# Performance work log

Measured on AMD Instinct MI355X. Metric: run time of the kernel, lower is better.

The kernel has to match this reference:

```python
import jax, jax.numpy as jnp
import numpy as np
jax.config.update('jax_enable_x64', True)

T = 524288      # hash table size (2^19)
D = 3           # input_dim
F = 2           # feature_dim
L = 16          # levels
N_MIN, N_MAX = 16, 512
B = 262144      # batch of query points
V = 2 ** D      # voxel corners

_b = np.exp((np.log(N_MAX) - np.log(N_MIN)) / (L - 1))
RESOLUTIONS = jnp.asarray(np.floor(N_MIN * _b ** np.arange(L)).astype(np.int64)).reshape(1, 1, L, 1)
PRIMES = jnp.asarray(np.array([1, 2654435761, 805459861], dtype=np.int64))
_border = np.empty((D, V), dtype=np.int64)
for i in range(D):
    _border[i, :] = np.array(([0] * 2 ** i + [1] * 2 ** i) * 2 ** (D - i - 1), dtype=np.int64)
BORDER_ADDS = jnp.asarray(_border).reshape(1, D, 1, V)


def setup_inputs() -> dict:
    key = jax.random.key(0)
    kx, kt = jax.random.split(key)
    x = jax.random.uniform(kx, (B, D), dtype=jnp.float32)  # coords in [0,1)
    # nn.Embedding init: uniform(-1e-4, 1e-4) per level
    tables = jax.random.uniform(kt, (L, T, F), dtype=jnp.float32, minval=-1e-4, maxval=1e-4)
    return {"x": x, "tables": tables}


def reference(x, tables):
    # scale to each grid resolution: (B, D, L, 1)
    scaled = x[:, :, None, None] * RESOLUTIONS.astype(x.dtype)
    # voxel corner integer coords: (B, D, L, V)
    grid = jnp.floor(scaled).astype(jnp.int64) + BORDER_ADDS
    # NVIDIA fast hash: xor of coord*prime over dims, mod T -> (B, L, V)
    hashed = grid * PRIMES.reshape(1, D, 1, 1)
    idx = jnp.remainder(jnp.bitwise_xor(jnp.bitwise_xor(hashed[:, 0], hashed[:, 1]), hashed[:, 2]), T)
    # gather per-level features: (B, L, V, F)
    feats = tables[jnp.arange(L)[None, :, None], idx]
    # multilinear interpolation weights: prod over dims -> (B, L, V)
    w = jnp.prod(1.0 - jnp.abs(scaled - grid.astype(scaled.dtype)), axis=1)
    # weighted corner sum -> (B, L, F) -> (B, L*F)
    out = jnp.einsum('blv,blvf->blf', w, feats)
    return out.reshape(x.shape[0], L * F)
```

## Files before the change

kernel.cpp:

```cpp
#include <hip/hip_runtime.h>


constexpr int      kT      = 524288;
constexpr unsigned kMask   = kT - 1;
constexpr int      kB      = 262144;
constexpr unsigned kP1     = 2654435761u;
constexpr unsigned kP2     = 805459861u;
constexpr int      kBins   = 4096;
constexpr int      kCap    = 128;
constexpr int      kOvfCap = 65536;

typedef float f32x4 __attribute__((ext_vector_type(4)));

__device__ __forceinline__ unsigned morton12(float x0, float x1, float x2) {
    unsigned a = min(15u, (unsigned)(x0 * 16.0f));
    unsigned b = min(15u, (unsigned)(x1 * 16.0f));
    unsigned c = min(15u, (unsigned)(x2 * 16.0f));
    unsigned key = 0;
#pragma unroll
    for (int i = 3; i >= 0; --i)
        key = (key << 3) | (((a >> i) & 1u) << 2) | (((b >> i) & 1u) << 1) | ((c >> i) & 1u);
    return key;
}

__device__ __forceinline__ void hashenc_body(const float x0, const float x1, const float x2,
                                             const f32x4* __restrict__ tab4base,
                                             f32x4* __restrict__ out, const unsigned sid) {
    f32x4 o[8];
    constexpr float kResF[16] = {16, 20, 25, 32, 40, 50, 64, 80,
                                 101, 128, 161, 203, 256, 322, 406, 512};
#pragma unroll
    for (int l = 0; l < 16; ++l) {
        const float res = kResF[l];
        const float s0 = x0 * res, s1 = x1 * res, s2 = x2 * res;
        const float f0 = floorf(s0), f1 = floorf(s1), f2 = floorf(s2);
        const float r0 = s0 - f0, r1 = s1 - f1, r2 = s2 - f2;
        const unsigned c0 = (unsigned)f0;
        const unsigned h1a = (unsigned)f1 * kP1, h1b = h1a + kP1;
        const unsigned h2a = (unsigned)f2 * kP2, h2b = h2a + kP2;
        const float w0a = 1.0f - r0, w1a = 1.0f - r1, w2a = 1.0f - r2;
        const f32x4* __restrict__ tab4 = tab4base + (size_t)l * (kT / 2);
        float a0 = 0.0f, a1 = 0.0f;
#pragma unroll
        for (int q = 0; q < 4; ++q) {
            const unsigned g = ((q & 1) ? h1b : h1a) ^ ((q & 2) ? h2b : h2a);
            const unsigned i0 = (c0 ^ g) & kMask;
            const unsigned i1 = ((c0 + 1u) ^ g) & kMask;
            const f32x4 A = tab4[i0 >> 1];
            const f32x4 B = tab4[i1 >> 1];
            const float p0x = (i0 & 1) ? A.z : A.x;
            const float p0y = (i0 & 1) ? A.w : A.y;
            const float p1x = (i1 & 1) ? B.z : B.x;
            const float p1y = (i1 & 1) ? B.w : B.y;
            const float wyz = ((q & 1) ? r1 : w1a) * ((q & 2) ? r2 : w2a);
            const float wl = wyz * w0a;
            const float wr = wyz * r0;
            a0 = fmaf(wl, p0x, fmaf(wr, p1x, a0));
            a1 = fmaf(wl, p0y, fmaf(wr, p1y, a1));
        }
        if (l & 1) { o[l >> 1].z = a0; o[l >> 1].w = a1; }
        else       { o[l >> 1].x = a0; o[l >> 1].y = a1; }
    }
    f32x4* op = out + (size_t)sid * 8;
#pragma unroll
    for (int k = 0; k < 8; ++k) __builtin_nontemporal_store(o[k], op + k);
}

__global__ __launch_bounds__(256) void scatter_kernel(const float* __restrict__ x,
                                                      unsigned* __restrict__ cnt,
                                                      f32x4* __restrict__ xsort,
                                                      f32x4* __restrict__ ovf) {
    const int i = blockIdx.x * 256 + threadIdx.x;
    const float x0 = x[3 * i], x1 = x[3 * i + 1], x2 = x[3 * i + 2];
    const unsigned key = morton12(x0, x1, x2);
    const unsigned slot = atomicAdd(&cnt[key], 1u);
    f32x4 v;
    v.x = x0; v.y = x1; v.z = x2; v.w = __uint_as_float((unsigned)i);
    if (slot < (unsigned)kCap) {
        xsort[key * kCap + slot] = v;
    } else {
        const unsigned o = atomicAdd(&cnt[kBins], 1u);
        if (o < (unsigned)kOvfCap) ovf[o] = v;
    }
}

__global__ __launch_bounds__(256) void hashenc_sorted(const f32x4* __restrict__ xsort,
                                                      const unsigned* __restrict__ cnt,
                                                      const f32x4* __restrict__ tab4base,
                                                      f32x4* __restrict__ out) {
    const int bid = (int)((blockIdx.x & 7) * 256 + (blockIdx.x >> 3));
    const int gs  = bid * 256 + (int)threadIdx.x;
    const int bin = gs >> 7;
    const int sl  = gs & (kCap - 1);
    const unsigned n = min(cnt[bin], (unsigned)kCap);
    if ((unsigned)sl >= n) return;
    const f32x4 v = xsort[gs];
    hashenc_body(v.x, v.y, v.z, tab4base, out, __float_as_uint(v.w));
}

__global__ __launch_bounds__(256) void cleanup_kernel(const f32x4* __restrict__ ovf,
                                                      const unsigned* __restrict__ cnt,
                                                      const f32x4* __restrict__ tab4base,
                                                      f32x4* __restrict__ out) {
    const unsigned oc = min(cnt[kBins], (unsigned)kOvfCap);
    for (unsigned j = threadIdx.x; j < oc; j += 256) {
        const f32x4 v = ovf[j];
        hashenc_body(v.x, v.y, v.z, tab4base, out, __float_as_uint(v.w));
    }
}

__global__ __launch_bounds__(256, 4) void hashenc_direct(const float* __restrict__ x,
                                                         const f32x4* __restrict__ tab4base,
                                                         f32x4* __restrict__ out) {
    const int i = blockIdx.x * 256 + threadIdx.x;
    hashenc_body(x[3 * i], x[3 * i + 1], x[3 * i + 2], tab4base, out, (unsigned)i);
}

extern "C" void kernel_launch(void* const* d_in, const int* in_sizes, int n_in,
                              void* d_out, int out_size, void* d_ws, size_t ws_size,
                              hipStream_t stream) {
    const float*  x    = (const float*)d_in[0];
    const f32x4*  tab4 = (const f32x4*)d_in[1];
    f32x4*        out  = (f32x4*)d_out;

    const size_t cntBytes   = (size_t)(kBins + 16) * 4;
    const size_t ovfBytes   = (size_t)kOvfCap * 16;
    const size_t xsortBytes = (size_t)kBins * kCap * 16;
    const size_t need = cntBytes + ovfBytes + xsortBytes;

    if (ws_size >= need) {
        unsigned* cnt   = (unsigned*)d_ws;
        f32x4*    ovf   = (f32x4*)((char*)d_ws + cntBytes);
        f32x4*    xsort = ovf + kOvfCap;
        hipMemsetAsync(cnt, 0, cntBytes, stream);
        scatter_kernel<<<kB / 256, 256, 0, stream>>>(x, cnt, xsort, ovf);
        hashenc_sorted<<<(kBins * kCap) / 256, 256, 0, stream>>>(xsort, cnt, tab4, out);
        cleanup_kernel<<<1, 256, 0, stream>>>(ovf, cnt, tab4, out);
    } else {
        hashenc_direct<<<kB / 256, 256, 0, stream>>>(x, tab4, out);
    }
}
```

Baseline: 157.2 us.

## Stage coarse-level hash corners per wavefront in LDS for Morton-binned points

For six of the coarse levels (0,1,2,3,4,6), each wavefront handling a spatial Morton bin cooperatively gathers every hash-table corner that bin can touch into LDS. Each point then interpolates those levels from LDS instead of issuing eight scattered global loads per level, which removes redundant gathers across points that share voxels. The remaining levels keep the direct gather. Invalid lanes now run with dummy coordinates so the whole wavefront can take part in the fill. The change adds per-wave fill work, LDS usage and no barrier (it relies on wavefront-synchronous LDS access), and the interpolation code contains a redundant, oddly written accumulation sequence.

Measured after the change: 155.4 us. Within noise of the previous version (-1.2%).

```diff
diff --git a/kernel.cpp b/kernel.cpp
--- a/kernel.cpp
+++ b/kernel.cpp
@@ -9,8 +9,10 @@
 constexpr int      kBins   = 4096;
 constexpr int      kCap    = 128;
 constexpr int      kOvfCap = 65536;
+constexpr int      kCoopTot = 413;
 
 typedef float f32x4 __attribute__((ext_vector_type(4)));
+typedef float f32x2 __attribute__((ext_vector_type(2)));
 
 __device__ __forceinline__ unsigned morton12(float x0, float x1, float x2) {
     unsigned a = min(15u, (unsigned)(x0 * 16.0f));
@@ -21,6 +23,38 @@
     for (int i = 3; i >= 0; --i)
         key = (key << 3) | (((a >> i) & 1u) << 2) | (((b >> i) & 1u) << 1) | ((c >> i) & 1u);
     return key;
+}
+
+__device__ __forceinline__ f32x2 direct_level(const float x0, const float x1, const float x2,
+                                              const float res,
+                                              const f32x4* __restrict__ tab4) {
+    const float s0 = x0 * res, s1 = x1 * res, s2 = x2 * res;
+    const float f0 = floorf(s0), f1 = floorf(s1), f2 = floorf(s2);
+    const float r0 = s0 - f0, r1 = s1 - f1, r2 = s2 - f2;
+    const unsigned c0 = (unsigned)f0;
+    const unsigned h1a = (unsigned)f1 * kP1, h1b = h1a + kP1;
+    const unsigned h2a = (unsigned)f2 * kP2, h2b = h2a + kP2;
+    const float w0a = 1.0f - r0, w1a = 1.0f - r1, w2a = 1.0f - r2;
+    float a0 = 0.0f, a1 = 0.0f;
+#pragma unroll
+    for (int q = 0; q < 4; ++q) {
+        const unsigned g = ((q & 1) ? h1b : h1a) ^ ((q & 2) ? h2b : h2a);
+        const unsigned i0 = (c0 ^ g) & kMask;
+        const unsigned i1 = ((c0 + 1u) ^ g) & kMask;
+        const f32x4 A = tab4[i0 >> 1];
+        const f32x4 B = tab4[i1 >> 1];
+        const float p0x = (i0 & 1) ? A.z : A.x;
+        const float p0y = (i0 & 1) ? A.w : A.y;
+        const float p1x = (i1 & 1) ? B.z : B.x;
+        const float p1y = (i1 & 1) ? B.w : B.y;
+        const float wyz = ((q & 1) ? r1 : w1a) * ((q & 2) ? r2 : w2a);
+        const float wl = wyz * w0a;
+        const float wr = wyz * r0;
+        a0 = fmaf(wl, p0x, fmaf(wr, p1x, a0));
+        a1 = fmaf(wl, p0y, fmaf(wr, p1y, a1));
+    }
+    f32x2 r; r.x = a0; r.y = a1;
+    return r;
 }
 
 __device__ __forceinline__ void hashenc_body(const float x0, const float x1, const float x2,
@@ -31,39 +65,71 @@
                                  101, 128, 161, 203, 256, 322, 406, 512};
 #pragma unroll
     for (int l = 0; l < 16; ++l) {
-        const float res = kResF[l];
-        const float s0 = x0 * res, s1 = x1 * res, s2 = x2 * res;
-        const float f0 = floorf(s0), f1 = floorf(s1), f2 = floorf(s2);
-        const float r0 = s0 - f0, r1 = s1 - f1, r2 = s2 - f2;
-        const unsigned c0 = (unsigned)f0;
-        const unsigned h1a = (unsigned)f1 * kP1, h1b = h1a + kP1;
-        const unsigned h2a = (unsigned)f2 * kP2, h2b = h2a + kP2;
-        const float w0a = 1.0f - r0, w1a = 1.0f - r1, w2a = 1.0f - r2;
-        const f32x4* __restrict__ tab4 = tab4base + (size_t)l * (kT / 2);
-        float a0 = 0.0f, a1 = 0.0f;
-#pragma unroll
-        for (int q = 0; q < 4; ++q) {
-            const unsigned g = ((q & 1) ? h1b : h1a) ^ ((q & 2) ? h2b : h2a);
-            const unsigned i0 = (c0 ^ g) & kMask;
-            const unsigned i1 = ((c0 + 1u) ^ g) & kMask;
-            const f32x4 A = tab4[i0 >> 1];
-            const f32x4 B = tab4[i1 >> 1];
-            const float p0x = (i0 & 1) ? A.z : A.x;
-            const float p0y = (i0 & 1) ? A.w : A.y;
-            const float p1x = (i1 & 1) ? B.z : B.x;
-            const float p1y = (i1 & 1) ? B.w : B.y;
-            const float wyz = ((q & 1) ? r1 : w1a) * ((q & 2) ? r2 : w2a);
-            const float wl = wyz * w0a;
-            const float wr = wyz * r0;
-            a0 = fmaf(wl, p0x, fmaf(wr, p1x, a0));
-            a1 = fmaf(wl, p0y, fmaf(wr, p1y, a1));
+        const f32x2 r = direct_level(x0, x1, x2, kResF[l], tab4base + (size_t)l * (kT / 2));
+        if (l & 1) { o[l >> 1].z = r.x; o[l >> 1].w = r.y; }
+        else       { o[l >> 1].x = r.x; o[l >> 1].y = r.y; }
+    }
+    f32x4* op = out + (size_t)sid * 8;
+#pragma unroll
+    for (int k = 0; k < 8; ++k) __builtin_nontemporal_store(o[k], op + k);
+}
+
+template <int L, int N, int RES, int OFF>
+__device__ __forceinline__ void coop_fill(const unsigned lane,
+                                          const unsigned bx, const unsigned by, const unsigned bz,
+                                          const f32x2* __restrict__ tab2,
+                                          f32x2* __restrict__ wlds) {
+    const unsigned lo0 = (bx * RES) >> 4, lo1 = (by * RES) >> 4, lo2 = (bz * RES) >> 4;
+    const unsigned h1 = lo1 * kP1, h2 = lo2 * kP2;
+    constexpr int NC = N * N * N;
+#pragma unroll
+    for (int k = 0; k < (NC + 63) / 64; ++k) {
+        const int t = (int)lane + 64 * k;
+        if (t < NC) {
+            const unsigned dx = (unsigned)t / (N * N);
+            const unsigned rem = (unsigned)t % (N * N);
+            const unsigned dy = rem / N, dz = rem % N;
+            const unsigned idx = ((lo0 + dx) ^ (h1 + dy * kP1) ^ (h2 + dz * kP2)) & kMask;
+            wlds[OFF + t] = tab2[(size_t)L * kT + idx];
         }
-        if (l & 1) { o[l >> 1].z = a0; o[l >> 1].w = a1; }
-        else       { o[l >> 1].x = a0; o[l >> 1].y = a1; }
-    }
-    f32x4* op = out + (size_t)sid * 8;
-#pragma unroll
-    for (int k = 0; k < 8; ++k) __builtin_nontemporal_store(o[k], op + k);
+    }
+}
+
+template <int N, int RES, int OFF>
+__device__ __forceinline__ f32x2 coop_interp(const float x0, const float x1, const float x2,
+                                             const unsigned bx, const unsigned by, const unsigned bz,
+                                             const f32x2* __restrict__ wlds) {
+    const float res = (float)RES;
+    const float s0 = x0 * res, s1 = x1 * res, s2 = x2 * res;
+    const float f0 = floorf(s0), f1 = floorf(s1), f2 = floorf(s2);
+    const float r0 = s0 - f0, r1 = s1 - f1, r2 = s2 - f2;
+    const unsigned lo0 = (bx * RES) >> 4, lo1 = (by * RES) >> 4, lo2 = (bz * RES) >> 4;
+    const unsigned i0 = min((unsigned)f0 - lo0, (unsigned)(N - 2));
+    const unsigned i1 = min((unsigned)f1 - lo1, (unsigned)(N - 2));
+    const unsigned i2 = min((unsigned)f2 - lo2, (unsigned)(N - 2));
+    const int s00 = OFF + (int)(i0 * (N * N) + i1 * N + i2);
+    const f32x2 c000 = wlds[s00],             c001 = wlds[s00 + 1];
+    const f32x2 c010 = wlds[s00 + N],         c011 = wlds[s00 + N + 1];
+    const f32x2 c100 = wlds[s00 + N * N],     c101 = wlds[s00 + N * N + 1];
+    const f32x2 c110 = wlds[s00 + N * N + N], c111 = wlds[s00 + N * N + N + 1];
+    const float w0a = 1.f - r0, w1a = 1.f - r1, w2a = 1.f - r2;
+    float a0, a1;
+    const float w00 = w0a * w1a, w01 = w0a * r1, w10 = r0 * w1a, w11 = r0 * r1;
+    a0 = w00 * w2a * c000.x; a1 = w00 * w2a * c000.y;
+    a0 = fmaf(w00 * r2, c001.x, a0); a1 = fmaf(w00 * r2, c001.y, a1);
+    a0 = fmaf(w01 * w2a, c010.x, a0); a1 = fmaf(w01 * w2a, c010.y, a1);
+    a0 = fmaf(w01 * r2, c011.x, a0); a1 = fmaf(w01 * r2, c011.y, a1);
+    a0 = fmaf(w10 * w2a, c100.x, a0); a1 = fmaf(w10 * w2a, c100.y, a1);
+    a0 = fmaf(w10 * r2, c101.x, a0); a1 = fmaf(w10 * r2, c101.y, a1);
+    a0 = fmaf(w11 * w2a, c110.x, a0); a1 = fmaf(w11 * r2 / r2 * r2, 0.f, a1);
+    a1 = fmaf(w11 * w2a, c110.y, fmaf(w10 * r2, c101.y, fmaf(w10 * w2a, c100.y,
+         fmaf(w01 * r2, c011.y, fmaf(w01 * w2a, c010.y, fmaf(w00 * r2, c001.y, w00 * w2a * c000.y))))));
+    a0 = fmaf(w11 * w2a, c110.x, fmaf(w10 * r2, c101.x, fmaf(w10 * w2a, c100.x,
+         fmaf(w01 * r2, c011.x, fmaf(w01 * w2a, c010.x, fmaf(w00 * r2, c001.x, w00 * w2a * c000.x))))));
+    a0 = fmaf(w11 * r2, c111.x, a0);
+    a1 = fmaf(w11 * r2, c111.y, a1);
+    f32x2 r; r.x = a0; r.y = a1;
+    return r;
 }
 
 __global__ __launch_bounds__(256) void scatter_kernel(const float* __restrict__ x,
@@ -86,16 +152,60 @@
 
 __global__ __launch_bounds__(256) void hashenc_sorted(const f32x4* __restrict__ xsort,
                                                       const unsigned* __restrict__ cnt,
+                                                      const f32x2* __restrict__ tab2,
                                                       const f32x4* __restrict__ tab4base,
                                                       f32x4* __restrict__ out) {
+    __shared__ f32x2 lds[4][kCoopTot];
+    const int tid = threadIdx.x;
     const int bid = (int)((blockIdx.x & 7) * 256 + (blockIdx.x >> 3));
-    const int gs  = bid * 256 + (int)threadIdx.x;
+    const int gs  = bid * 256 + tid;
     const int bin = gs >> 7;
     const int sl  = gs & (kCap - 1);
     const unsigned n = min(cnt[bin], (unsigned)kCap);
-    if ((unsigned)sl >= n) return;
+    if ((unsigned)(sl & 64) >= n) return;
+    const bool valid = (unsigned)sl < n;
     const f32x4 v = xsort[gs];
-    hashenc_body(v.x, v.y, v.z, tab4base, out, __float_as_uint(v.w));
+    const float x0 = valid ? v.x : 0.5f;
+    const float x1 = valid ? v.y : 0.5f;
+    const float x2 = valid ? v.z : 0.5f;
+
+    const unsigned key = (unsigned)bin;
+    const unsigned bx = ((key >> 2) & 1) | ((key >> 4) & 2) | ((key >> 6) & 4) | ((key >> 8) & 8);
+    const unsigned by = ((key >> 1) & 1) | ((key >> 3) & 2) | ((key >> 5) & 4) | ((key >> 7) & 8);
+    const unsigned bz = ((key     ) & 1) | ((key >> 2) & 2) | ((key >> 4) & 4) | ((key >> 6) & 8);
+
+    f32x2* wlds = lds[tid >> 6];
+    const unsigned lane = (unsigned)(tid & 63);
+    coop_fill<0, 2, 16, 0>(lane, bx, by, bz, tab2, wlds);
+    coop_fill<1, 4, 20, 8>(lane, bx, by, bz, tab2, wlds);
+    coop_fill<2, 4, 25, 72>(lane, bx, by, bz, tab2, wlds);
+    coop_fill<3, 3, 32, 136>(lane, bx, by, bz, tab2, wlds);
+    coop_fill<4, 5, 40, 163>(lane, bx, by, bz, tab2, wlds);
+    coop_fill<6, 5, 64, 288>(lane, bx, by, bz, tab2, wlds);
+
+    f32x4 o[8];
+    { const f32x2 r = direct_level(x0, x1, x2, 50.f,  tab4base + (size_t)5  * (kT / 2)); o[2].z = r.x; o[2].w = r.y; }
+    { const f32x2 r = direct_level(x0, x1, x2, 80.f,  tab4base + (size_t)7  * (kT / 2)); o[3].z = r.x; o[3].w = r.y; }
+    { const f32x2 r = direct_level(x0, x1, x2, 101.f, tab4base + (size_t)8  * (kT / 2)); o[4].x = r.x; o[4].y = r.y; }
+    { const f32x2 r = direct_level(x0, x1, x2, 128.f, tab4base + (size_t)9  * (kT / 2)); o[4].z = r.x; o[4].w = r.y; }
+    { const f32x2 r = direct_level(x0, x1, x2, 161.f, tab4base + (size_t)10 * (kT / 2)); o[5].x = r.x; o[5].y = r.y; }
+    { const f32x2 r = direct_level(x0, x1, x2, 203.f, tab4base + (size_t)11 * (kT / 2)); o[5].z = r.x; o[5].w = r.y; }
+    { const f32x2 r = direct_level(x0, x1, x2, 256.f, tab4base + (size_t)12 * (kT / 2)); o[6].x = r.x; o[6].y = r.y; }
+    { const f32x2 r = direct_level(x0, x1, x2, 322.f, tab4base + (size_t)13 * (kT / 2)); o[6].z = r.x; o[6].w = r.y; }
+    { const f32x2 r = direct_level(x0, x1, x2, 406.f, tab4base + (size_t)14 * (kT / 2)); o[7].x = r.x; o[7].y = r.y; }
+    { const f32x2 r = direct_level(x0, x1, x2, 512.f, tab4base + (size_t)15 * (kT / 2)); o[7].z = r.x; o[7].w = r.y; }
+    { const f32x2 r = coop_interp<2, 16, 0>(x0, x1, x2, bx, by, bz, wlds);   o[0].x = r.x; o[0].y = r.y; }
+    { const f32x2 r = coop_interp<4, 20, 8>(x0, x1, x2, bx, by, bz, wlds);   o[0].z = r.x; o[0].w = r.y; }
+    { const f32x2 r = coop_interp<4, 25, 72>(x0, x1, x2, bx, by, bz, wlds);  o[1].x = r.x; o[1].y = r.y; }
+    { const f32x2 r = coop_interp<3, 32, 136>(x0, x1, x2, bx, by, bz, wlds); o[1].z = r.x; o[1].w = r.y; }
+    { const f32x2 r = coop_interp<5, 40, 163>(x0, x1, x2, bx, by, bz, wlds); o[2].x = r.x; o[2].y = r.y; }
+    { const f32x2 r = coop_interp<5, 64, 288>(x0, x1, x2, bx, by, bz, wlds); o[3].x = r.x; o[3].y = r.y; }
+
+    if (valid) {
+        f32x4* op = out + (size_t)__float_as_uint(v.w) * 8;
+#pragma unroll
+        for (int k = 0; k < 8; ++k) __builtin_nontemporal_store(o[k], op + k);
+    }
 }
 
 __global__ __launch_bounds__(256) void cleanup_kernel(const f32x4* __restrict__ ovf,
@@ -120,6 +230,7 @@
                               void* d_out, int out_size, void* d_ws, size_t ws_size,
                               hipStream_t stream) {
     const float*  x    = (const float*)d_in[0];
+    const f32x2*  tab2 = (const f32x2*)d_in[1];
     const f32x4*  tab4 = (const f32x4*)d_in[1];
     f32x4*        out  = (f32x4*)d_out;
 
@@ -134,7 +245,7 @@
         f32x4*    xsort = ovf + kOvfCap;
         hipMemsetAsync(cnt, 0, cntBytes, stream);
         scatter_kernel<<<kB / 256, 256, 0, stream>>>(x, cnt, xsort, ovf);
-        hashenc_sorted<<<(kBins * kCap) / 256, 256, 0, stream>>>(xsort, cnt, tab4, out);
+        hashenc_sorted<<<(kBins * kCap) / 256, 256, 0, stream>>>(xsort, cnt, tab2, tab4, out);
         cleanup_kernel<<<1, 256, 0, stream>>>(ovf, cnt, tab4, out);
     } else {
         hashenc_direct<<<kB / 256, 256, 0, stream>>>(x, tab4, out);
```
